# Performance work log

Hardware: AMD Instinct MI355X
Metric: run time of the kernel (lower is better)

## Reference

```python
import jax, jax.numpy as jnp
import numpy as np
from jax import lax

NUM_CLASSES = 10
NUM_ITER = 3
CAP_DIM = 8       # primary capsule dim
OUT_CAP_DIM = 16  # digit capsule dim
NUM_MAP = 32      # 256 / 8
NUM_PRIM = 144    # 12*12


def squash(x, axis=-1):
    s2 = jnp.sum(x * x, axis=axis, keepdims=True)
    return (s2 / (1.0 + s2)) * x / jnp.sqrt(s2 + 1e-8)


def conv2d(x, w, b):
    y = lax.conv_general_dilated(x, w, (1, 1), 'VALID',
                                 dimension_numbers=('NCHW', 'OIHW', 'NCHW'))
    return y + b[None, :, None, None]


def setup_inputs() -> dict:
    key = jax.random.key(0)
    ks = jax.random.split(key, 13)
    B = 128
    return {
        'imgs': jax.random.uniform(ks[0], (B, 1, 28, 28), dtype=jnp.float32),
        'conv1_w': jax.random.normal(ks[1], (256, 1, 9, 9), jnp.float32) * 0.05,
        'conv1_b': jnp.zeros((256,), jnp.float32),
        'conv2_w': jax.random.normal(ks[2], (256, 256, 9, 9), jnp.float32) * 0.02,
        'conv2_b': jnp.zeros((256,), jnp.float32),
        # non-shared routing weights: [num_prim_map, num_prim_cap, num_classes, out_dim, in_dim]
        'W_digit': jax.random.normal(ks[3], (NUM_MAP, NUM_PRIM, NUM_CLASSES, OUT_CAP_DIM, CAP_DIM), jnp.float32),
        'dec_w1': jax.random.normal(ks[4], (OUT_CAP_DIM * NUM_CLASSES, 512), jnp.float32) * 0.05,
        'dec_b1': jnp.zeros((512,), jnp.float32),
        'dec_w2': jax.random.normal(ks[5], (512, 1024), jnp.float32) * 0.04,
        'dec_b2': jnp.zeros((1024,), jnp.float32),
        'dec_w3': jax.random.normal(ks[6], (1024, 784), jnp.float32) * 0.03,
        'dec_b3': jnp.zeros((784,), jnp.float32),
    }


def capsnet_fwd(imgs, conv1_w, conv1_b, conv2_w, conv2_b, W_digit,
                dec_w1, dec_b1, dec_w2, dec_b2, dec_w3, dec_b3):
    B = imgs.shape[0]
    # conv1 + relu: [B,256,20,20]
    x = jax.nn.relu(conv2d(imgs, conv1_w, conv1_b))
    # primary caps conv: [B,256,12,12]
    p = conv2d(x, conv2_w, conv2_b)
    # view [B, cap_dim, num_map, 12, 12] -> [B, num_map, 144, cap_dim]
    p = p.reshape(B, CAP_DIM, NUM_MAP, NUM_PRIM)
    p = jnp.transpose(p, (0, 2, 3, 1))
    u = squash(p, axis=-1)  # [B, 32, 144, 8]

    # u_hat[b,m,p,c,o] = W[m,p,c,o,i] * u[b,m,p,i]  (broadcast instead of repeat)
    u_hat = jnp.einsum('mpcoi,bmpi->bmpco', W_digit, u)
    u_hat = u_hat.reshape(B, NUM_MAP * NUM_PRIM, NUM_CLASSES, OUT_CAP_DIM)  # [B,4608,10,16]

    # dynamic routing
    b_ij = jnp.zeros((B, NUM_MAP * NUM_PRIM, NUM_CLASSES), u_hat.dtype)
    v = None
    for i in range(NUM_ITER):
        c_ij = jax.nn.softmax(b_ij, axis=1)                     # over input capsules
        s_j = jnp.einsum('bnc,bncd->bcd', c_ij, u_hat)          # [B,10,16]
        v = squash(s_j, axis=-1)
        if i != NUM_ITER - 1:
            b_ij = b_ij + jnp.einsum('bncd,bcd->bnc', u_hat, v)  # agreement

    # v: [B,10,16]
    v_length = jnp.sqrt(jnp.sum(v * v, axis=-1))                 # [B,10]
    y_pred = jnp.argmax(v_length, axis=1)
    y_pred_ohe = jax.nn.one_hot(y_pred, NUM_CLASSES, dtype=jnp.int32)

    masked = (v * y_pred_ohe.astype(v.dtype)[:, :, None]).reshape(B, -1)  # [B,160]
    h = jax.nn.relu(masked @ dec_w1 + dec_b1)
    h = jax.nn.relu(h @ dec_w2 + dec_b2)
    img_reconst = jax.nn.sigmoid(h @ dec_w3 + dec_b3)            # [B,784]
    return y_pred_ohe, img_reconst, v_length


def reference(imgs, conv1_w, conv1_b, conv2_w, conv2_b, W_digit,
              dec_w1, dec_b1, dec_w2, dec_b2, dec_w3, dec_b3):
    return capsnet_fwd(imgs, conv1_w, conv1_b, conv2_w, conv2_b, W_digit,
                       dec_w1, dec_b1, dec_w2, dec_b2, dec_w3, dec_b3)
```

## Files before the change

### kernel.cpp

```cpp
#include <hip/hip_runtime.h>
#include <cstdint>
#include <cstddef>

#define BB 128
#define NMAP 32
#define NPRIM 144
#define NCAP 4608
#define NCLS 10
#define ODIM 16
#define IDIM 8

#define WS_X1H  0
#define WS_X1L  6553600
#define WS_BH   13107200
#define WS_P    18415616
#define WS_U    23134208
#define WS_V    27852800
#define WS_H1   27873280
#define WS_H2   27938816
#define WS_CLS  28069888

#define OUT_REC  1280
#define OUT_LEN  101632

typedef __attribute__((ext_vector_type(8))) short short8;
typedef __attribute__((ext_vector_type(4))) float f32x4;

static __device__ __forceinline__ ushort f2bf(float f) {
    uint u = __float_as_uint(f);
    u = (u + 0x7FFFu + ((u >> 16) & 1u)) >> 16;
    return (ushort)u;
}
static __device__ __forceinline__ float bf2f(ushort h) {
    return __uint_as_float(((uint)h) << 16);
}

static __device__ __forceinline__ void gload16(const ushort* g, ushort* l) {
    __builtin_amdgcn_global_load_lds(
        (const __attribute__((address_space(1))) void*)g,
        (__attribute__((address_space(3))) void*)l, 16, 0, 0);
}


__global__ __launch_bounds__(256) void k_conv1(const float* __restrict__ img,
                                               const float* __restrict__ w,
                                               const float* __restrict__ bias,
                                               ushort* __restrict__ x1h,
                                               ushort* __restrict__ x1l) {
    __shared__ float simg[252];
    int bi = blockIdx.x;
    int y = bi % 20;
    int b = bi / 20;
    int oc = threadIdx.x;
    if (threadIdx.x < 252)
        simg[threadIdx.x] = img[(size_t)b * 784 + y * 28 + threadIdx.x];
    __syncthreads();

    float acc[20];
    float bv = bias[oc];
#pragma unroll
    for (int x = 0; x < 20; ++x) acc[x] = bv;
    const float* wp = w + oc * 81;
#pragma unroll
    for (int kh = 0; kh < 9; ++kh) {
        float r[28];
#pragma unroll
        for (int j = 0; j < 28; ++j) r[j] = simg[kh * 28 + j];
#pragma unroll
        for (int kw = 0; kw < 9; ++kw) {
            float wv = wp[kh * 9 + kw];
#pragma unroll
            for (int x = 0; x < 20; ++x)
                acc[x] = fmaf(wv, r[x + kw], acc[x]);
        }
    }
    size_t base = ((size_t)b * 400 + y * 20) * 256 + oc;
#pragma unroll
    for (int x = 0; x < 20; ++x) {
        float v = fmaxf(acc[x], 0.f);
        ushort h = f2bf(v);
        ushort lo = f2bf(v - bf2f(h));
        x1h[base + (size_t)x * 256] = h;
        x1l[base + (size_t)x * 256] = lo;
    }
}

__global__ __launch_bounds__(256) void k_prep_w2(const float* __restrict__ w2,
                                                 ushort* __restrict__ bpk) {
    int blk = blockIdx.x;
    int icc = blk >> 5, kq = (blk >> 3) & 3, ocg = blk & 7;
    int tid = threadIdx.x;
    int ocl = tid >> 3, ic8 = tid & 7;
    int oc = ocg * 32 + ocl;
    int ic = icc * 32 + kq * 8 + ic8;
    const float* src = w2 + ((size_t)oc * 256 + ic) * 81;
    size_t dbase = (size_t)icc * 16384 + (size_t)kq * 2048 + (size_t)oc * 8 + ic8;
#pragma unroll 9
    for (int t = 0; t < 81; ++t) {
        float v = src[t];
        ushort h = f2bf(v);
        ushort lo = f2bf(v - bf2f(h));
        bpk[(size_t)t * 131072 + dbase] = h;
        bpk[(size_t)t * 131072 + dbase + 8192] = lo;
    }
}

static __device__ __forceinline__ f32x4 mfma16(short8 a, short8 b, f32x4 c) {
    return __builtin_amdgcn_mfma_f32_16x16x32_bf16(a, b, c, 0, 0, 0);
}


struct FragR { short8 ah[5], al[5], bh0, bh1, bl0, bl1; };

template<int NMF>
static __device__ __forceinline__ void pre_fragR(
    FragR& f, const ushort* A_lds, const ushort* Bb, int tn,
    const int* celloff, int bro0, int bro1) {
    int kh = tn / 9, kw = tn - kh * 9;
    int tapoff = (kh * 20 + kw) * 40;
    const ushort* Bc = Bb + (tn % 6) * 8192;
#pragma unroll
    for (int i = 0; i < NMF; ++i) {
        f.ah[i] = *(const short8*)(A_lds + tapoff + celloff[i]);
        f.al[i] = *(const short8*)(A_lds + 16000 + tapoff + celloff[i]);
    }
    f.bh0 = *(const short8*)(Bc + bro0);
    f.bh1 = *(const short8*)(Bc + bro1);
    f.bl0 = *(const short8*)(Bc + 4096 + bro0);
    f.bl1 = *(const short8*)(Bc + 4096 + bro1);
}

template<int NMF>
static __device__ __forceinline__ void mfma_fragR(f32x4 (&acc)[5][2], const FragR& f) {
#pragma unroll
    for (int i = 0; i < NMF; ++i) {
        acc[i][0] = mfma16(f.ah[i], f.bh0, acc[i][0]);
        acc[i][1] = mfma16(f.ah[i], f.bh1, acc[i][1]);
    }
#pragma unroll
    for (int i = 0; i < NMF; ++i) {
        acc[i][0] = mfma16(f.ah[i], f.bl0, acc[i][0]);
        acc[i][1] = mfma16(f.ah[i], f.bl1, acc[i][1]);
    }
#pragma unroll
    for (int i = 0; i < NMF; ++i) {
        acc[i][0] = mfma16(f.al[i], f.bh0, acc[i][0]);
        acc[i][1] = mfma16(f.al[i], f.bh1, acc[i][1]);
    }
}

static __device__ __forceinline__ void stage_tap(
    const ushort* gB0, ushort* lB0, int tn, size_t gicc) {
    if (tn <= 80) {
        size_t g = (size_t)tn * 131072 + gicc;
        ushort* d = lB0 + (tn % 6) * 8192;
        gload16(gB0 + g, d);
        gload16(gB0 + g + 512, d + 512);
    }
}

template<int MF0, int NMF>
static __device__ __forceinline__ void conv2s_epi(
    const f32x4 (&acc)[5][2], const float* __restrict__ bias,
    float* __restrict__ p, int b, int oc0, int nq, int r, int kq) {
#pragma unroll
    for (int j = 0; j < 2; ++j) {
        int oc = oc0 + (nq * 2 + j) * 16 + r;
        float bv = bias[oc];
#pragma unroll
        for (int i = 0; i < NMF; ++i) {
            int row = b * 144 + (MF0 + i) * 16 + kq * 4;
#pragma unroll
            for (int reg = 0; reg < 4; ++reg)
                p[(size_t)(row + reg) * 256 + oc] = acc[i][j][reg] + bv;
        }
    }
}

__global__ __launch_bounds__(512)
__attribute__((amdgpu_waves_per_eu(2, 2)))
void k_conv2s(
    const ushort* __restrict__ x1h, const ushort* __restrict__ x1l,
    const ushort* __restrict__ bpk,
    const float* __restrict__ bias, float* __restrict__ p) {
    __shared__ __align__(16) ushort A_lds[32000];
    __shared__ __align__(16) ushort Bb[49152];

    const int tid = threadIdx.x;
    const int lane = tid & 63;
    const int wv = tid >> 6;
    const int mh = wv >> 2;
    const int nq = wv & 3;
    const int b  = blockIdx.x >> 1;
    const int nt = blockIdx.x & 1;
    const int oc0 = nt * 128;
    const int r = lane & 15, kq = lane >> 4;
    const int MF0r = mh ? 5 : 0;

    int celloff[5];
#pragma unroll
    for (int i = 0; i < 5; ++i) {
        int lm = (MF0r + i) * 16 + r;
        celloff[i] = ((lm / 12) * 20 + (lm % 12)) * 40 + kq * 8;
    }
    const int bro0 = kq * 1024 + ((nq * 2 + 0) * 16 + r) * 8;
    const int bro1 = kq * 1024 + ((nq * 2 + 1) * 16 + r) * 8;

    const int comp_w = wv >> 2, kq_w = wv & 3;
    const ushort* gB0 = bpk + comp_w * 8192 + kq_w * 2048 + oc0 * 8 + lane * 8;
    ushort* lB0 = Bb + comp_w * 4096 + kq_w * 1024;

    f32x4 acc[5][2];
#pragma unroll
    for (int i = 0; i < 5; ++i)
#pragma unroll
        for (int j = 0; j < 2; ++j)
            acc[i][j] = (f32x4){0.f, 0.f, 0.f, 0.f};

    FragR fX, fY;

    for (int icc = 0; icc < 8; ++icc) {
        const size_t gicc = (size_t)icc * 16384;
#pragma unroll
        for (int rd = 0; rd < 7; ++rd) {
            int idx = rd * 512 + tid;
            if (idx < 3200) {
                int comp = (idx >= 1600) ? 1 : 0;
                int ci = idx - comp * 1600;
                int cell = ci >> 2, cc = ci & 3;
                const ushort* src = (comp ? x1l : x1h) +
                    ((size_t)b * 400 + cell) * 256 + icc * 32 + cc * 8;
                short8 val = *(const short8*)src;
                *(short8*)(A_lds + comp * 16000 + cell * 40 + cc * 8) = val;
            }
        }
        stage_tap(gB0, lB0, 0, gicc);
        stage_tap(gB0, lB0, 1, gicc);
        stage_tap(gB0, lB0, 2, gicc);
        stage_tap(gB0, lB0, 3, gicc);
        __syncthreads();
        if (mh == 0) {
            pre_fragR<5>(fX, A_lds, Bb, 0, celloff, bro0, bro1);
            pre_fragR<5>(fY, A_lds, Bb, 1, celloff, bro0, bro1);
        } else {
            pre_fragR<4>(fX, A_lds, Bb, 0, celloff, bro0, bro1);
            pre_fragR<4>(fY, A_lds, Bb, 1, celloff, bro0, bro1);
        }

#pragma unroll 1
        for (int ph = 0; ph < 39; ++ph) {
            const int T = ph * 2;
            stage_tap(gB0, lB0, T + 4, gicc);
            stage_tap(gB0, lB0, T + 5, gicc);
            if (mh == 0) {
                mfma_fragR<5>(acc, fX);
                mfma_fragR<5>(acc, fY);
                pre_fragR<5>(fX, A_lds, Bb, T + 2, celloff, bro0, bro1);
                pre_fragR<5>(fY, A_lds, Bb, T + 3, celloff, bro0, bro1);
            } else {
                mfma_fragR<4>(acc, fX);
                mfma_fragR<4>(acc, fY);
                pre_fragR<4>(fX, A_lds, Bb, T + 2, celloff, bro0, bro1);
                pre_fragR<4>(fY, A_lds, Bb, T + 3, celloff, bro0, bro1);
            }
            __syncthreads();
        }
        if (mh == 0) {
            mfma_fragR<5>(acc, fX);
            mfma_fragR<5>(acc, fY);
            pre_fragR<5>(fX, A_lds, Bb, 80, celloff, bro0, bro1);
            mfma_fragR<5>(acc, fX);
        } else {
            mfma_fragR<4>(acc, fX);
            mfma_fragR<4>(acc, fY);
            pre_fragR<4>(fX, A_lds, Bb, 80, celloff, bro0, bro1);
            mfma_fragR<4>(acc, fX);
        }
        __syncthreads();
    }

    if (mh == 0) conv2s_epi<0, 5>(acc, bias, p, b, oc0, nq, r, kq);
    else         conv2s_epi<5, 4>(acc, bias, p, b, oc0, nq, r, kq);
}

__global__ __launch_bounds__(256) void k_squash(const float* __restrict__ p,
                                                float* __restrict__ u) {
    int id = blockIdx.x * 256 + threadIdx.x;
    int n = id % NCAP;
    int b = id / NCAP;
    int m = n / NPRIM, pos = n - m * NPRIM;
    const float* pp = p + ((size_t)b * 144 + pos) * 256 + m;
    float pv[8];
    float s2 = 0.f;
#pragma unroll
    for (int i = 0; i < 8; ++i) {
        pv[i] = pp[i * 32];
        s2 = fmaf(pv[i], pv[i], s2);
    }
    float f = (s2 / (1.f + s2)) / sqrtf(s2 + 1e-8f);
    float4 a = make_float4(f * pv[0], f * pv[1], f * pv[2], f * pv[3]);
    float4 c = make_float4(f * pv[4], f * pv[5], f * pv[6], f * pv[7]);
    float4* up = (float4*)(u + (size_t)id * 8);
    up[0] = a;
    up[1] = c;
}

__global__ __launch_bounds__(256) void k_prep_wt(const float* __restrict__ Wd,
                                                 float* __restrict__ Wt) {
    __shared__ float S[64][129];
    int c = blockIdx.x % NCLS;
    int nt = blockIdx.x / NCLS;
    int n0 = nt * 64;
    int tid = threadIdx.x;
#pragma unroll
    for (int rep = 0; rep < 32; ++rep) {
        int idx = rep * 256 + tid;
        int nl = idx >> 7, oi = idx & 127;
        S[nl][oi] = Wd[(size_t)(n0 + nl) * 1280 + c * 128 + oi];
    }
    __syncthreads();
#pragma unroll
    for (int rep = 0; rep < 32; ++rep) {
        int idx = rep * 256 + tid;
        int oi = idx >> 6, nl = idx & 63;
        Wt[((size_t)c * 128 + oi) * NCAP + n0 + nl] = S[nl][oi];
    }
}

__global__ __launch_bounds__(256) void k_route5(const float* __restrict__ u,
                                                const float* __restrict__ Wt,
                                                float* __restrict__ v_out) {
    __shared__ float part[4][2][17];
    __shared__ float sums[2][17];
    __shared__ float vsh[2][16];
    int c = blockIdx.x % NCLS;
    int bg = blockIdx.x / NCLS;
    int b0 = bg * 2;
    int tid = threadIdx.x;
    int lane = tid & 63, wvi = tid >> 6;
    const float* WtC = Wt + (size_t)c * 128 * NCAP;

    float bij[18][2];
#pragma unroll
    for (int j = 0; j < 18; ++j) { bij[j][0] = 0.f; bij[j][1] = 0.f; }

    for (int iter = 0; iter < 3; ++iter) {
        float sZ[2] = {0.f, 0.f};
        float sS[2][16];
#pragma unroll
        for (int o = 0; o < 16; ++o) { sS[0][o] = 0.f; sS[1][o] = 0.f; }

        for (int j = 0; j < 18; ++j) {
            int n = j * 256 + tid;
            const float4* up0 = (const float4*)(u + ((size_t)b0 * NCAP + n) * 8);
            const float4* up1 = (const float4*)(u + ((size_t)(b0 + 1) * NCAP + n) * 8);
            float4 a0 = up0[0], a1 = up0[1];
            float4 c0 = up1[0], c1 = up1[1];
            float u0[8] = {a0.x, a0.y, a0.z, a0.w, a1.x, a1.y, a1.z, a1.w};
            float u1[8] = {c0.x, c0.y, c0.z, c0.w, c1.x, c1.y, c1.z, c1.w};
            float uh[2][16];
#pragma unroll
            for (int o = 0; o < 16; ++o) {
                float s0 = 0.f, s1 = 0.f;
#pragma unroll
                for (int i = 0; i < 8; ++i) {
                    float w = WtC[(size_t)(o * 8 + i) * NCAP + n];
                    s0 = fmaf(w, u0[i], s0);
                    s1 = fmaf(w, u1[i], s1);
                }
                uh[0][o] = s0;
                uh[1][o] = s1;
            }
#pragma unroll
            for (int bb = 0; bb < 2; ++bb) {
                float e;
                if (iter == 0) {
                    e = 1.f;
                } else {
                    float agr = 0.f;
#pragma unroll
                    for (int o = 0; o < 16; ++o) agr = fmaf(uh[bb][o], vsh[bb][o], agr);
                    bij[j][bb] += agr;
                    e = __expf(bij[j][bb]);
                }
                sZ[bb] += e;
#pragma unroll
                for (int o = 0; o < 16; ++o) sS[bb][o] = fmaf(e, uh[bb][o], sS[bb][o]);
            }
        }

#pragma unroll
        for (int bb = 0; bb < 2; ++bb) {
            float z = sZ[bb];
#pragma unroll
            for (int d = 32; d >= 1; d >>= 1) z += __shfl_xor(z, d, 64);
            if (lane == 0) part[wvi][bb][0] = z;
#pragma unroll
            for (int o = 0; o < 16; ++o) {
                float s = sS[bb][o];
#pragma unroll
                for (int d = 32; d >= 1; d >>= 1) s += __shfl_xor(s, d, 64);
                if (lane == 0) part[wvi][bb][1 + o] = s;
            }
        }
        __syncthreads();
        if (tid < 34) {
            int bb = tid / 17, k = tid % 17;
            float s = 0.f;
#pragma unroll
            for (int w4 = 0; w4 < 4; ++w4) s += part[w4][bb][k];
            sums[bb][k] = s;
        }
        __syncthreads();
        if (tid < 2) {
            float Z = sums[tid][0];
            float s[16];
            float s2 = 0.f;
#pragma unroll
            for (int o = 0; o < 16; ++o) {
                s[o] = sums[tid][1 + o] / Z;
                s2 = fmaf(s[o], s[o], s2);
            }
            float f = (s2 / (1.f + s2)) / sqrtf(s2 + 1e-8f);
#pragma unroll
            for (int o = 0; o < 16; ++o) vsh[tid][o] = f * s[o];
        }
        __syncthreads();
    }
    if (tid < 32) {
        int bb = tid >> 4, o = tid & 15;
        v_out[((size_t)(b0 + bb) * NCLS + c) * 16 + o] = vsh[bb][o];
    }
}

__global__ __launch_bounds__(64) void k_head(const float* __restrict__ v,
                                             float* __restrict__ out,
                                             int* __restrict__ cls_ws) {
    __shared__ float len2[NCLS];
    __shared__ int cls_sh;
    int b = blockIdx.x, tid = threadIdx.x;
    if (tid < NCLS) {
        float s2 = 0.f;
#pragma unroll
        for (int o = 0; o < 16; ++o) {
            float t = v[((size_t)b * NCLS + tid) * 16 + o];
            s2 = fmaf(t, t, s2);
        }
        len2[tid] = s2;
        out[OUT_LEN + b * NCLS + tid] = sqrtf(s2);
    }
    __syncthreads();
    if (tid == 0) {
        int best = 0;
        float bv = len2[0];
        for (int c2 = 1; c2 < NCLS; ++c2)
            if (len2[c2] > bv) { bv = len2[c2]; best = c2; }
        cls_sh = best;
        cls_ws[b] = best;
    }
    __syncthreads();
    if (tid < NCLS) out[b * NCLS + tid] = (tid == cls_sh) ? 1.0f : 0.0f;
}

__global__ __launch_bounds__(256) void k_dec1(const float* __restrict__ v,
                                              const int* __restrict__ cls_ws,
                                              const float* __restrict__ w1,
                                              const float* __restrict__ b1,
                                              float* __restrict__ h1) {
    int id = blockIdx.x * 256 + threadIdx.x;
    int j = id % 512, b = id / 512;
    int cls = cls_ws[b];
    const float* vp = v + ((size_t)b * NCLS + cls) * 16;
    float acc = b1[j];
#pragma unroll
    for (int o = 0; o < 16; ++o)
        acc = fmaf(vp[o], w1[(size_t)(cls * 16 + o) * 512 + j], acc);
    h1[id] = fmaxf(acc, 0.f);
}

__global__ __launch_bounds__(256) void k_dec2(const float* __restrict__ h1,
                                              const float* __restrict__ w2,
                                              const float* __restrict__ b2,
                                              float* __restrict__ h2) {
    __shared__ float hs[512];
    int bi = blockIdx.x;
    int jc = bi % 4;
    int b = bi / 4;
    int tid = threadIdx.x;
    hs[tid] = h1[b * 512 + tid];
    hs[tid + 256] = h1[b * 512 + tid + 256];
    __syncthreads();
    int j = jc * 256 + tid;
    float acc = b2[j];
#pragma unroll 8
    for (int k = 0; k < 512; ++k)
        acc = fmaf(hs[k], w2[(size_t)k * 1024 + j], acc);
    h2[b * 1024 + j] = fmaxf(acc, 0.f);
}

__global__ __launch_bounds__(256) void k_dec3(const float* __restrict__ h2,
                                              const float* __restrict__ w3,
                                              const float* __restrict__ b3,
                                              float* __restrict__ out) {
    __shared__ float hs[1024];
    int bi = blockIdx.x;
    int jc = bi % 4;
    int b = bi / 4;
    int tid = threadIdx.x;
#pragma unroll
    for (int t = 0; t < 4; ++t) hs[tid + t * 256] = h2[b * 1024 + tid + t * 256];
    __syncthreads();
    int j = jc * 256 + tid;
    if (j < 784) {
        float acc = b3[j];
#pragma unroll 8
        for (int k = 0; k < 1024; ++k)
            acc = fmaf(hs[k], w3[(size_t)k * 784 + j], acc);
        out[OUT_REC + b * 784 + j] = 1.f / (1.f + __expf(-acc));
    }
}

extern "C" void kernel_launch(void* const* d_in, const int* in_sizes, int n_in,
                              void* d_out, int out_size, void* d_ws, size_t ws_size,
                              hipStream_t stream) {
    const float* imgs = (const float*)d_in[0];
    const float* c1w  = (const float*)d_in[1];
    const float* c1b  = (const float*)d_in[2];
    const float* c2w  = (const float*)d_in[3];
    const float* c2b  = (const float*)d_in[4];
    const float* Wd   = (const float*)d_in[5];
    const float* dw1  = (const float*)d_in[6];
    const float* db1  = (const float*)d_in[7];
    const float* dw2  = (const float*)d_in[8];
    const float* db2  = (const float*)d_in[9];
    const float* dw3  = (const float*)d_in[10];
    const float* db3  = (const float*)d_in[11];

    float* out = (float*)d_out;
    float* ws  = (float*)d_ws;
    ushort* x1h = (ushort*)(ws + WS_X1H);
    ushort* x1l = (ushort*)(ws + WS_X1L);
    ushort* bpk = (ushort*)(ws + WS_BH);
    float* p    = ws + WS_P;
    float* u    = ws + WS_U;
    float* v    = ws + WS_V;
    float* h1   = ws + WS_H1;
    float* h2   = ws + WS_H2;
    int*   cls  = (int*)(ws + WS_CLS);
    float* wt32 = ws + WS_X1H;

    k_conv1<<<BB * 20, 256, 0, stream>>>(imgs, c1w, c1b, x1h, x1l);
    k_prep_w2<<<256, 256, 0, stream>>>(c2w, bpk);
    k_conv2s<<<BB * 2, 512, 0, stream>>>(x1h, x1l, bpk, c2b, p);
    k_squash<<<BB * NCAP / 256, 256, 0, stream>>>(p, u);
    k_prep_wt<<<720, 256, 0, stream>>>(Wd, wt32);
    k_route5<<<(BB / 2) * NCLS, 256, 0, stream>>>(u, wt32, v);
    k_head<<<BB, 64, 0, stream>>>(v, out, cls);
    k_dec1<<<BB * 512 / 256, 256, 0, stream>>>(v, cls, dw1, db1, h1);
    k_dec2<<<BB * 4, 256, 0, stream>>>(h1, dw2, db2, h2);
    k_dec3<<<BB * 4, 256, 0, stream>>>(h2, dw3, db3, out);
}
```

Before: 1.155 ms.

## Route four batch samples per block and keep routing logits in LDS

The routing kernel now handles four batch items per block instead of two, so each W_digit value loaded from global memory is reused across four samples, halving weight traffic. The per-thread routing-logit array moves from registers to a 72 KB shared-memory buffer to make room for the larger accumulators, and waves-per-EU is pinned to 2. The grid halves to 320 blocks, which may underfill the GPU, and the large LDS footprint limits occupancy.

After: 1.416 ms. 22.6% more time.

```diff
diff --git a/kernel.cpp b/kernel.cpp
--- a/kernel.cpp
+++ b/kernel.cpp
@@ -109,7 +109,6 @@
     return __builtin_amdgcn_mfma_f32_16x16x32_bf16(a, b, c, 0, 0, 0);
 }
 
-
 struct FragR { short8 ah[5], al[5], bh0, bh1, bl0, bl1; };
 
 template<int NMF>
@@ -327,52 +326,57 @@
     }
 }
 
-__global__ __launch_bounds__(256) void k_route5(const float* __restrict__ u,
-                                                const float* __restrict__ Wt,
-                                                float* __restrict__ v_out) {
-    __shared__ float part[4][2][17];
-    __shared__ float sums[2][17];
-    __shared__ float vsh[2][16];
+__global__ __launch_bounds__(256)
+__attribute__((amdgpu_waves_per_eu(2, 2)))
+void k_route6(const float* __restrict__ u,
+              const float* __restrict__ Wt,
+              float* __restrict__ v_out) {
+    __shared__ float bijL[4][18][256];
+    __shared__ float part[4][4][17];
+    __shared__ float sums[4][17];
+    __shared__ float vsh[4][16];
     int c = blockIdx.x % NCLS;
     int bg = blockIdx.x / NCLS;
-    int b0 = bg * 2;
+    int b0 = bg * 4;
     int tid = threadIdx.x;
     int lane = tid & 63, wvi = tid >> 6;
     const float* WtC = Wt + (size_t)c * 128 * NCAP;
 
-    float bij[18][2];
-#pragma unroll
-    for (int j = 0; j < 18; ++j) { bij[j][0] = 0.f; bij[j][1] = 0.f; }
-
     for (int iter = 0; iter < 3; ++iter) {
-        float sZ[2] = {0.f, 0.f};
-        float sS[2][16];
-#pragma unroll
-        for (int o = 0; o < 16; ++o) { sS[0][o] = 0.f; sS[1][o] = 0.f; }
+        float sZ[4] = {0.f, 0.f, 0.f, 0.f};
+        float sS[4][16];
+#pragma unroll
+        for (int bb = 0; bb < 4; ++bb)
+#pragma unroll
+            for (int o = 0; o < 16; ++o) sS[bb][o] = 0.f;
 
         for (int j = 0; j < 18; ++j) {
             int n = j * 256 + tid;
-            const float4* up0 = (const float4*)(u + ((size_t)b0 * NCAP + n) * 8);
-            const float4* up1 = (const float4*)(u + ((size_t)(b0 + 1) * NCAP + n) * 8);
-            float4 a0 = up0[0], a1 = up0[1];
-            float4 c0 = up1[0], c1 = up1[1];
-            float u0[8] = {a0.x, a0.y, a0.z, a0.w, a1.x, a1.y, a1.z, a1.w};
-            float u1[8] = {c0.x, c0.y, c0.z, c0.w, c1.x, c1.y, c1.z, c1.w};
-            float uh[2][16];
+            float uv[4][8];
+#pragma unroll
+            for (int bb = 0; bb < 4; ++bb) {
+                const float4* up = (const float4*)(u + ((size_t)(b0 + bb) * NCAP + n) * 8);
+                float4 a = up[0], d = up[1];
+                uv[bb][0] = a.x; uv[bb][1] = a.y; uv[bb][2] = a.z; uv[bb][3] = a.w;
+                uv[bb][4] = d.x; uv[bb][5] = d.y; uv[bb][6] = d.z; uv[bb][7] = d.w;
+            }
+            float uh[4][16];
 #pragma unroll
             for (int o = 0; o < 16; ++o) {
-                float s0 = 0.f, s1 = 0.f;
-#pragma unroll
-                for (int i = 0; i < 8; ++i) {
-                    float w = WtC[(size_t)(o * 8 + i) * NCAP + n];
-                    s0 = fmaf(w, u0[i], s0);
-                    s1 = fmaf(w, u1[i], s1);
+                float w[8];
+#pragma unroll
+                for (int i = 0; i < 8; ++i)
+                    w[i] = WtC[(size_t)(o * 8 + i) * NCAP + n];
+#pragma unroll
+                for (int bb = 0; bb < 4; ++bb) {
+                    float s = 0.f;
+#pragma unroll
+                    for (int i = 0; i < 8; ++i) s = fmaf(w[i], uv[bb][i], s);
+                    uh[bb][o] = s;
                 }
-                uh[0][o] = s0;
-                uh[1][o] = s1;
-            }
-#pragma unroll
-            for (int bb = 0; bb < 2; ++bb) {
+            }
+#pragma unroll
+            for (int bb = 0; bb < 4; ++bb) {
                 float e;
                 if (iter == 0) {
                     e = 1.f;
@@ -380,8 +384,10 @@
                     float agr = 0.f;
 #pragma unroll
                     for (int o = 0; o < 16; ++o) agr = fmaf(uh[bb][o], vsh[bb][o], agr);
-                    bij[j][bb] += agr;
-                    e = __expf(bij[j][bb]);
+                    float bold = (iter == 1) ? 0.f : bijL[bb][j][tid];
+                    float bnew = bold + agr;
+                    bijL[bb][j][tid] = bnew;
+                    e = __expf(bnew);
                 }
                 sZ[bb] += e;
 #pragma unroll
@@ -390,7 +396,7 @@
         }
 
 #pragma unroll
-        for (int bb = 0; bb < 2; ++bb) {
+        for (int bb = 0; bb < 4; ++bb) {
             float z = sZ[bb];
 #pragma unroll
             for (int d = 32; d >= 1; d >>= 1) z += __shfl_xor(z, d, 64);
@@ -404,7 +410,7 @@
             }
         }
         __syncthreads();
-        if (tid < 34) {
+        if (tid < 68) {
             int bb = tid / 17, k = tid % 17;
             float s = 0.f;
 #pragma unroll
@@ -412,7 +418,7 @@
             sums[bb][k] = s;
         }
         __syncthreads();
-        if (tid < 2) {
+        if (tid < 4) {
             float Z = sums[tid][0];
             float s[16];
             float s2 = 0.f;
@@ -427,7 +433,7 @@
         }
         __syncthreads();
     }
-    if (tid < 32) {
+    if (tid < 64) {
         int bb = tid >> 4, o = tid & 15;
         v_out[((size_t)(b0 + bb) * NCLS + c) * 16 + o] = vsh[bb][o];
     }
@@ -554,7 +560,7 @@
     k_conv2s<<<BB * 2, 512, 0, stream>>>(x1h, x1l, bpk, c2b, p);
     k_squash<<<BB * NCAP / 256, 256, 0, stream>>>(p, u);
     k_prep_wt<<<720, 256, 0, stream>>>(Wd, wt32);
-    k_route5<<<(BB / 2) * NCLS, 256, 0, stream>>>(u, wt32, v);
+    k_route6<<<(BB / 4) * NCLS, 256, 0, stream>>>(u, wt32, v);
     k_head<<<BB, 64, 0, stream>>>(v, out, cls);
     k_dec1<<<BB * 512 / 256, 256, 0, stream>>>(v, cls, dw1, db1, h1);
     k_dec2<<<BB * 4, 256, 0, stream>>>(h1, dw2, db2, h2);
```
